# Kernel tuning notes

Hardware: AMD Instinct MI355X
Metric: run time of the kernel (lower is better)

The kernel has to match this reference:

```python
import jax, jax.numpy as jnp
import numpy as np

SAMPLES = 16        # samples per spatial dim -> M = SAMPLES**2 sample points
SAMPLE_PAD = 0
K = 9               # nearest neighbors == conv kernel size == stride


def setup_inputs() -> dict:
    key = jax.random.key(0)
    k1, k2, k3 = jax.random.split(key, 3)
    B, C, H, W = 16, 128, 64, 64
    OUT = 128
    x = jax.random.normal(k1, (B, C, H, W), dtype=jnp.float32)
    w = jax.random.normal(k2, (OUT, C, K), dtype=jnp.float32) * 0.05
    b = jax.random.normal(k3, (OUT,), dtype=jnp.float32) * 0.05
    return {"x": x, "w": w, "b": b}


def reference(x, w, b):
    B, C, H, W = x.shape
    N = H * W
    # --- spatial sample grid (static, shape-derived) ---
    xi = jnp.round(jnp.linspace(SAMPLE_PAD, H - SAMPLE_PAD - 1, SAMPLES)).astype(jnp.int32)
    yi = jnp.round(jnp.linspace(SAMPLE_PAD, W - SAMPLE_PAD - 1, SAMPLES)).astype(jnp.int32)
    xg, yg = jnp.meshgrid(xi, yi, indexing='ij')
    x_sample = x[:, :, xg, yg].reshape(B, C, -1)          # (B, C, M)
    x1 = x.reshape(B, C, N)                                # (B, C, N)
    # --- squared Euclidean distance between tokens and samples ---
    dots = jnp.einsum('bcn,bcm->bnm', x1, x_sample)        # (B, N, M)
    n2 = jnp.sum(x1 * x1, axis=1)                          # (B, N)
    m2 = jnp.sum(x_sample * x_sample, axis=1)              # (B, M)
    dist2 = n2[:, :, None] + m2[:, None, :] - 2.0 * dots   # (B, N, M)
    # K nearest samples per token (smallest distance)
    _, idx = jax.lax.top_k(-dist2, K)                      # (B, N, K) int32
    # gather neighbor features from the sample set: (B, C, N, K)
    nbrs = jnp.take_along_axis(x_sample[:, :, None, :],
                               idx[:, None, :, :], axis=3)
    # Conv1d(kernel=K, stride=K) over the (B, C, N*K) prime tensor
    out = jnp.einsum('bcnk,ock->bon', nbrs, w) + b[None, :, None]
    return out.reshape(B, w.shape[0], H, W)
```

## Files before the change

kernel.cpp:

```cpp
#include <hip/hip_runtime.h>

#define NB   16
#define NC   128
#define NN   4096
#define NM   256
#define NK   9
#define NO   128

typedef __attribute__((ext_vector_type(8))) short bf16x8;
typedef __attribute__((ext_vector_type(4))) float f32x4;

__device__ __constant__ int d_grid16[16] = {0,4,8,13,17,21,25,29,34,38,42,46,50,55,59,63};

__device__ inline unsigned short bf16_rne(float v) {
    unsigned u = __float_as_uint(v);
    return (unsigned short)((u + 0x7FFFu + ((u >> 16) & 1u)) >> 16);
}

__device__ __forceinline__ void merge16(unsigned* s, const unsigned* q) {
    unsigned r[16];
    #pragma unroll
    for (int i = 0; i < 16; ++i) r[i] = min(s[i], q[15 - i]);
    #pragma unroll
    for (int d = 8; d >= 1; d >>= 1)
        #pragma unroll
        for (int i = 0; i < 16; ++i)
            if (!(i & d)) { unsigned a = r[i], b2 = r[i + d]; r[i] = min(a, b2); r[i + d] = max(a, b2); }
    #pragma unroll
    for (int i = 0; i < 16; ++i) s[i] = r[i];
}

__global__ __launch_bounds__(256) void k_prep(const float* __restrict__ x,
                                              const float* __restrict__ w,
                                              float* __restrict__ xsT,
                                              unsigned short* __restrict__ xsTh,
                                              unsigned short* __restrict__ xsTl,
                                              unsigned short* __restrict__ Wth,
                                              unsigned short* __restrict__ Wtl,
                                              float* __restrict__ n2g,
                                              float* __restrict__ m2) {
    __shared__ float tile[16 * 260];
    int bx = blockIdx.x, t = threadIdx.x;
    if (bx < 128) {
        int b = bx >> 3, c0 = (bx & 7) * 16;
        int m = t;
        int pix = d_grid16[m >> 4] * 64 + d_grid16[m & 15];
        #pragma unroll
        for (int cc = 0; cc < 16; ++cc)
            tile[cc * 260 + m] = x[((size_t)b * NC + c0 + cc) * NN + pix];
        __syncthreads();
        #pragma unroll
        for (int e = 0; e < 4; ++e) {
            float fv[4];
            fv[0] = tile[(4 * e + 0) * 260 + m];
            fv[1] = tile[(4 * e + 1) * 260 + m];
            fv[2] = tile[(4 * e + 2) * 260 + m];
            fv[3] = tile[(4 * e + 3) * 260 + m];
            size_t base = ((size_t)b * NM + m) * NC + c0 + 4 * e;
            *(float4*)&xsT[base] = make_float4(fv[0], fv[1], fv[2], fv[3]);
            unsigned short h4[4], l4[4];
            #pragma unroll
            for (int e2 = 0; e2 < 4; ++e2) {
                unsigned short h = bf16_rne(fv[e2]);
                h4[e2] = h;
                l4[e2] = bf16_rne(fv[e2] - __uint_as_float(((unsigned)h) << 16));
            }
            *(ushort4*)&xsTh[base] = make_ushort4(h4[0], h4[1], h4[2], h4[3]);
            *(ushort4*)&xsTl[base] = make_ushort4(l4[0], l4[1], l4[2], l4[3]);
        }
    } else if (bx < 704) {
        int f = (bx - 128) * 256 + t;
        int ko = f >> 7, c = f & 127;
        int o = ko & 127, k = ko >> 7;
        float v = w[(size_t)o * 1152 + c * 9 + k];
        unsigned short h = bf16_rne(v);
        Wth[f] = h;
        Wtl[f] = bf16_rne(v - __uint_as_float(((unsigned)h) << 16));
    } else if (bx < 960) {
        #pragma clang fp contract(off)
        int i = bx - 704;
        int b = i >> 4, n = (i & 15) * 256 + t;
        const float* p = x + (size_t)b * NC * NN + n;
        float a = 0.f;
        #pragma unroll 16
        for (int c = 0; c < NC; ++c) { float v = p[(size_t)c * NN]; a = __fadd_rn(a, __fmul_rn(v, v)); }
        n2g[(size_t)b * NN + n] = a;
    } else {
        #pragma clang fp contract(off)
        int b = bx - 960;
        int pix = d_grid16[t >> 4] * 64 + d_grid16[t & 15];
        const float* p = x + (size_t)b * NC * NN + pix;
        float a = 0.f;
        #pragma unroll 16
        for (int c = 0; c < NC; ++c) { float v = p[(size_t)c * NN]; a = __fadd_rn(a, __fmul_rn(v, v)); }
        m2[b * NM + t] = a;
    }
}

__global__ __launch_bounds__(256) void k_g(const unsigned short* __restrict__ xsTh,
                                           const unsigned short* __restrict__ xsTl,
                                           const unsigned short* __restrict__ Wth,
                                           const unsigned short* __restrict__ Wtl,
                                           float* __restrict__ G) {
    int id = blockIdx.x;
    int b = id & 15, r = id >> 4;
    int kk = r % 9, q = r / 9;
    int mt = q >> 1, jh = q & 1;
    int t = threadIdx.x;
    int w = t >> 6, lane = t & 63;
    int lr = lane & 15, quad = lane >> 4;
    int m = b * NM + mt * 64 + w * 16 + lr;
    const unsigned short* aph = xsTh + (size_t)m * NC;
    const unsigned short* apl = xsTl + (size_t)m * NC;
    f32x4 acc[4];
    #pragma unroll
    for (int j = 0; j < 4; ++j) acc[j] = (f32x4){0.f, 0.f, 0.f, 0.f};
    #pragma unroll
    for (int kb = 0; kb < 4; ++kb) {
        int co = kb * 32 + quad * 8;
        bf16x8 Ah = *(const bf16x8*)&aph[co];
        bf16x8 Al = *(const bf16x8*)&apl[co];
        #pragma unroll
        for (int j = 0; j < 4; ++j) {
            size_t wrow = ((size_t)kk * 128 + jh * 64 + 16 * j + lr) * NC + co;
            bf16x8 Bh = *(const bf16x8*)&Wth[wrow];
            bf16x8 Bl = *(const bf16x8*)&Wtl[wrow];
            acc[j] = __builtin_amdgcn_mfma_f32_16x16x32_bf16(Ah, Bh, acc[j], 0, 0, 0);
            acc[j] = __builtin_amdgcn_mfma_f32_16x16x32_bf16(Al, Bh, acc[j], 0, 0, 0);
            acc[j] = __builtin_amdgcn_mfma_f32_16x16x32_bf16(Ah, Bl, acc[j], 0, 0, 0);
        }
    }
    int mrow = b * NM + mt * 64 + w * 16 + quad * 4;
    #pragma unroll
    for (int j = 0; j < 4; ++j)
        #pragma unroll
        for (int r2 = 0; r2 < 4; ++r2)
            G[((size_t)(mrow + r2)) * 1152 + kk * 128 + jh * 64 + 16 * j + lr] = acc[j][r2];
}

__global__ __launch_bounds__(256, 2) void k_sel(const float* __restrict__ x,
                                                const unsigned short* __restrict__ xsTh,
                                                const unsigned short* __restrict__ xsTl,
                                                const float* __restrict__ m2,
                                                int* __restrict__ idx) {
    __shared__ __align__(16) unsigned short xhp[32 * 136];
    __shared__ __align__(16) unsigned short xlp[32 * 136];
    __shared__ __align__(16) unsigned wl[2 * 4 * 16 * 16];
    __shared__ float m2l[256];

    int b = blockIdx.x & 15, n0 = (blockIdx.x >> 4) * 32;
    int t = threadIdx.x;
    int w = t >> 6, lane = t & 63;
    int lr = lane & 15, quad = lane >> 4;

    m2l[t] = m2[b * NM + t];

    #pragma unroll
    for (int it = 0; it < 4; ++it) {
        int f4 = it * 256 + t;
        int c = f4 >> 3, nn4 = (f4 & 7) * 4;
        float4 v = *(const float4*)&x[((size_t)b * NC + c) * NN + n0 + nn4];
        float vf[4] = {v.x, v.y, v.z, v.w};
        #pragma unroll
        for (int e = 0; e < 4; ++e) {
            unsigned short h = bf16_rne(vf[e]);
            unsigned short l = bf16_rne(vf[e] - __uint_as_float(((unsigned)h) << 16));
            xhp[(nn4 + e) * 136 + c] = h;
            xlp[(nn4 + e) * 136 + c] = l;
        }
    }
    __syncthreads();

    f32x4 acc[2][4];
    #pragma unroll
    for (int i = 0; i < 2; ++i)
        #pragma unroll
        for (int j = 0; j < 4; ++j) acc[i][j] = (f32x4){0.f, 0.f, 0.f, 0.f};
    int mbase = w * 64;
    #pragma unroll
    for (int kb = 0; kb < 4; ++kb) {
        int co = kb * 32 + quad * 8;
        bf16x8 Bh0 = *(const bf16x8*)&xhp[lr * 136 + co];
        bf16x8 Bl0 = *(const bf16x8*)&xlp[lr * 136 + co];
        bf16x8 Bh1 = *(const bf16x8*)&xhp[(16 + lr) * 136 + co];
        bf16x8 Bl1 = *(const bf16x8*)&xlp[(16 + lr) * 136 + co];
        bf16x8 Ah[4], Al[4];
        #pragma unroll
        for (int j = 0; j < 4; ++j) {
            size_t arow = ((size_t)(b * NM + mbase + 16 * j + lr)) * NC + co;
            Ah[j] = *(const bf16x8*)&xsTh[arow];
            Al[j] = *(const bf16x8*)&xsTl[arow];
        }
        #pragma unroll
        for (int j = 0; j < 4; ++j) {
            acc[0][j] = __builtin_amdgcn_mfma_f32_16x16x32_bf16(Ah[j], Bh0, acc[0][j], 0, 0, 0);
            acc[0][j] = __builtin_amdgcn_mfma_f32_16x16x32_bf16(Ah[j], Bl0, acc[0][j], 0, 0, 0);
            acc[0][j] = __builtin_amdgcn_mfma_f32_16x16x32_bf16(Al[j], Bh0, acc[0][j], 0, 0, 0);
            acc[1][j] = __builtin_amdgcn_mfma_f32_16x16x32_bf16(Ah[j], Bh1, acc[1][j], 0, 0, 0);
            acc[1][j] = __builtin_amdgcn_mfma_f32_16x16x32_bf16(Ah[j], Bl1, acc[1][j], 0, 0, 0);
            acc[1][j] = __builtin_amdgcn_mfma_f32_16x16x32_bf16(Al[j], Bh1, acc[1][j], 0, 0, 0);
        }
    }

    unsigned s16v[16];
    int hfirst = 1 - (w & 1);
    #pragma unroll
    for (int hh = 0; hh < 2; ++hh) {
        int h = (hh == 0) ? hfirst : 1 - hfirst;
        #pragma unroll
        for (int j = 0; j < 4; ++j)
            #pragma unroll
            for (int r = 0; r < 4; ++r) {
                int m = mbase + 16 * j + quad * 4 + r;
                float key = fmaf(-2.f, acc[h][j][r], m2l[m]);
                unsigned u = __float_as_uint(key);
                u = (u & 0x80000000u) ? ~u : (u | 0x80000000u);
                s16v[4 * j + r] = (u & 0xFFFFFF00u) | (unsigned)m;
            }
        #define CE(i,jx) { unsigned a_ = s16v[i], b_ = s16v[jx]; s16v[i] = min(a_, b_); s16v[jx] = max(a_, b_); }
        CE(0,1) CE(2,3) CE(0,2) CE(1,3) CE(1,2)
        CE(4,5) CE(6,7) CE(4,6) CE(5,7) CE(5,6)
        CE(0,4) CE(2,6) CE(2,4) CE(1,5) CE(3,7) CE(3,5) CE(1,2) CE(3,4) CE(5,6)
        CE(8,9) CE(10,11) CE(8,10) CE(9,11) CE(9,10)
        CE(12,13) CE(14,15) CE(12,14) CE(13,15) CE(13,14)
        CE(8,12) CE(10,14) CE(10,12) CE(9,13) CE(11,15) CE(11,13) CE(9,10) CE(11,12) CE(13,14)
        CE(0,8) CE(4,12) CE(4,8) CE(2,10) CE(6,14) CE(6,10) CE(2,4) CE(6,8) CE(10,12)
        CE(1,9) CE(5,13) CE(5,9) CE(3,11) CE(7,15) CE(7,11) CE(3,5) CE(7,9) CE(11,13)
        CE(1,2) CE(3,4) CE(5,6) CE(7,8) CE(9,10) CE(11,12) CE(13,14)
        #undef CE

        #pragma unroll
        for (int d = 16; d <= 32; d <<= 1) {
            unsigned q[16];
            #pragma unroll
            for (int i = 0; i < 16; ++i) q[i] = (unsigned)__shfl_xor((int)s16v[i], d, 64);
            merge16(s16v, q);
        }
        if (quad == 0) {
            #pragma unroll
            for (int ii = 0; ii < 4; ++ii)
                *(uint4*)&wl[(((h * 4 + w) * 16 + lr) * 16) + 4 * ii] =
                    make_uint4(s16v[4*ii], s16v[4*ii+1], s16v[4*ii+2], s16v[4*ii+3]);
        }
    }
    __syncthreads();

    if (w < 2) {
        int h = w;
        #pragma unroll
        for (int p = 1; p < 4; ++p) {
            int pw = (w + p) & 3;
            unsigned q[16];
            #pragma unroll
            for (int i = 0; i < 16; ++i) q[i] = wl[(((h * 4 + pw) * 16 + lr) * 16) + i];
            merge16(s16v, q);
        }
        if (quad == 0) {
            int tok = 16 * h + lr;
            size_t obase = (size_t)(b * NN + n0 + tok) * NK;
            #pragma unroll
            for (int i = 0; i < 4; ++i)
                idx[obase + i] = (int)((s16v[4*i] & 255u) | ((s16v[4*i+1] & 255u) << 8) |
                                       ((s16v[4*i+2] & 255u) << 16) | ((s16v[4*i+3] & 255u) << 24));
        }
    }
}

__global__ __launch_bounds__(256) void k_out(const float* __restrict__ x,
                                             const float* __restrict__ xsT,
                                             const float* __restrict__ m2,
                                             const float* __restrict__ n2g,
                                             const float* __restrict__ G,
                                             const int* __restrict__ idx,
                                             const float* __restrict__ bias,
                                             float* __restrict__ out) {
    #pragma clang fp contract(off)
    __shared__ __align__(16) unsigned char ubuf[33792];
    __shared__ unsigned long long pairs[64 * 17];
    __shared__ int   idxl[576];
    __shared__ float m2l[256];
    __shared__ float n2l[64];
    __shared__ float biasl[128];
    float* xr = (float*)ubuf;
    float* S  = (float*)ubuf;

    int b = blockIdx.x & 15, n0 = (blockIdx.x >> 4) * 64;
    int t = threadIdx.x;

    m2l[t] = m2[b * NM + t];
    if (t < 64)  n2l[t] = n2g[(size_t)b * NN + n0 + t];
    if (t < 128) biasl[t] = bias[t];

    int tok = t >> 2, grp = t & 3;
    unsigned candw = (unsigned)idx[(size_t)(b * NN + n0 + tok) * NK + grp];

    #pragma unroll
    for (int it = 0; it < 8; ++it) {
        int f4 = it * 256 + t;
        int c = f4 >> 4, nn4 = (f4 & 15) * 4;
        float4 v = *(const float4*)&x[((size_t)b * NC + c) * NN + n0 + nn4];
        xr[(nn4 + 0) * 132 + c] = v.x;
        xr[(nn4 + 1) * 132 + c] = v.y;
        xr[(nn4 + 2) * 132 + c] = v.z;
        xr[(nn4 + 3) * 132 + c] = v.w;
    }
    __syncthreads();

    {
        float n2 = n2l[tok];
        int mym[4];
        unsigned long long myp[4];
        #pragma unroll
        for (int s = 0; s < 4; ++s) {
            int m = (int)((candw >> (8 * s)) & 255u);
            mym[s] = m;
            const float* xt = xsT + ((size_t)(b * NM + m)) * NC;
            float dot = 0.f;
            for (int c4 = 0; c4 < 32; ++c4) {
                float4 xv = *(const float4*)&xr[tok * 132 + 4 * c4];
                float4 sv = *(const float4*)&xt[4 * c4];
                dot = __fadd_rn(dot, __fmul_rn(xv.x, sv.x));
                dot = __fadd_rn(dot, __fmul_rn(xv.y, sv.y));
                dot = __fadd_rn(dot, __fmul_rn(xv.z, sv.z));
                dot = __fadd_rn(dot, __fmul_rn(xv.w, sv.w));
            }
            float key = __fsub_rn(__fadd_rn(n2, m2l[m]), __fmul_rn(2.f, dot));
            unsigned u = __float_as_uint(key);
            u = (u & 0x80000000u) ? ~u : (u | 0x80000000u);
            myp[s] = ((unsigned long long)u << 32) | (unsigned)mym[s];
            pairs[tok * 17 + grp * 4 + s] = myp[s];
        }
        __syncthreads();
        unsigned long long pl[16];
        #pragma unroll
        for (int l2 = 0; l2 < 16; ++l2) pl[l2] = pairs[tok * 17 + l2];
        #pragma unroll
        for (int s = 0; s < 4; ++s) {
            int rank = 0;
            #pragma unroll
            for (int l2 = 0; l2 < 16; ++l2) rank += (pl[l2] < myp[s]);
            if (rank < 9) idxl[tok * 9 + rank] = mym[s];
        }
    }
    __syncthreads();

    {
        int o = t & 127, half = t >> 7;
        for (int p = 0; p < 32; ++p) {
            int n = p * 2 + half;
            float a = biasl[o];
            #pragma unroll
            for (int k = 0; k < 9; ++k) {
                int m = idxl[n * 9 + k];
                a += G[(((size_t)(b * NM + m)) * NK + k) * 128 + o];
            }
            S[n * 129 + o] = a;
        }
    }
    __syncthreads();

    {
        int nn = t & 63, ob = t >> 6;
        for (int p = 0; p < 32; ++p) {
            int o2 = p * 4 + ob;
            out[((size_t)(b * NO + o2)) * NN + n0 + nn] = S[nn * 129 + o2];
        }
    }
}

extern "C" void kernel_launch(void* const* d_in, const int* in_sizes, int n_in,
                              void* d_out, int out_size, void* d_ws, size_t ws_size,
                              hipStream_t stream) {
    const float* x    = (const float*)d_in[0];
    const float* w    = (const float*)d_in[1];
    const float* bias = (const float*)d_in[2];
    float* out = (float*)d_out;

    float* ws   = (float*)d_ws;
    float* m2   = ws;
    float* n2g  = ws + 4096;
    float* xsT  = ws + 69632;
    float* G    = ws + 593920;
    int*   idx  = (int*)(ws + 5312512);
    unsigned short* xsTh = (unsigned short*)(ws + 5902336);
    unsigned short* xsTl = (unsigned short*)(ws + 6164480);
    unsigned short* Wth  = (unsigned short*)(ws + 6426624);
    unsigned short* Wtl  = (unsigned short*)(ws + 6500352);

    k_prep<<<dim3(976),  dim3(256), 0, stream>>>(x, w, xsT, xsTh, xsTl, Wth, Wtl, n2g, m2);
    k_g   <<<dim3(1152), dim3(256), 0, stream>>>(xsTh, xsTl, Wth, Wtl, G);
    k_sel <<<dim3(2048), dim3(256), 0, stream>>>(x, xsTh, xsTl, m2, idx);
    k_out <<<dim3(1024), dim3(256), 0, stream>>>(x, xsT, m2, n2g, G, idx, bias, out);
}
```

Measured before the change: 266.3 us.

## Alias shared buffers, shuffle candidate exchange, unroll refine dot, raise k_out occupancy

In k_sel, the bf16 input planes and the warp merge buffer now share one LDS allocation, with a barrier added before the merge phase reuses it. This shrinks shared memory per block. In k_out, the 16 candidate pairs per token are exchanged with wave shuffles instead of an LDS array plus a barrier. The exact-precision dot loop is fully unrolled to batch its loads, and the launch bounds request 4 blocks per CU. The aim is more resident blocks and fewer syncs, at the risk of register pressure from the unrolling and the occupancy hint.

```diff
diff --git a/kernel.cpp b/kernel.cpp
--- a/kernel.cpp
+++ b/kernel.cpp
@@ -143,10 +143,11 @@
                                                 const unsigned short* __restrict__ xsTl,
                                                 const float* __restrict__ m2,
                                                 int* __restrict__ idx) {
-    __shared__ __align__(16) unsigned short xhp[32 * 136];
-    __shared__ __align__(16) unsigned short xlp[32 * 136];
-    __shared__ __align__(16) unsigned wl[2 * 4 * 16 * 16];
+    __shared__ __align__(16) unsigned short planes[2 * 32 * 136];
     __shared__ float m2l[256];
+    unsigned short* xhp = planes;
+    unsigned short* xlp = planes + 32 * 136;
+    unsigned* wl = (unsigned*)planes;
 
     int b = blockIdx.x & 15, n0 = (blockIdx.x >> 4) * 32;
     int t = threadIdx.x;
@@ -201,6 +202,7 @@
             acc[1][j] = __builtin_amdgcn_mfma_f32_16x16x32_bf16(Al[j], Bh1, acc[1][j], 0, 0, 0);
         }
     }
+    __syncthreads();
 
     unsigned s16v[16];
     int hfirst = 1 - (w & 1);
@@ -266,17 +268,16 @@
     }
 }
 
-__global__ __launch_bounds__(256) void k_out(const float* __restrict__ x,
-                                             const float* __restrict__ xsT,
-                                             const float* __restrict__ m2,
-                                             const float* __restrict__ n2g,
-                                             const float* __restrict__ G,
-                                             const int* __restrict__ idx,
-                                             const float* __restrict__ bias,
-                                             float* __restrict__ out) {
+__global__ __launch_bounds__(256, 4) void k_out(const float* __restrict__ x,
+                                                const float* __restrict__ xsT,
+                                                const float* __restrict__ m2,
+                                                const float* __restrict__ n2g,
+                                                const float* __restrict__ G,
+                                                const int* __restrict__ idx,
+                                                const float* __restrict__ bias,
+                                                float* __restrict__ out) {
     #pragma clang fp contract(off)
     __shared__ __align__(16) unsigned char ubuf[33792];
-    __shared__ unsigned long long pairs[64 * 17];
     __shared__ int   idxl[576];
     __shared__ float m2l[256];
     __shared__ float n2l[64];
@@ -310,30 +311,48 @@
         float n2 = n2l[tok];
         int mym[4];
         unsigned long long myp[4];
+        const float4* xr4 = (const float4*)&xr[tok * 132];
         #pragma unroll
         for (int s = 0; s < 4; ++s) {
             int m = (int)((candw >> (8 * s)) & 255u);
             mym[s] = m;
-            const float* xt = xsT + ((size_t)(b * NM + m)) * NC;
+            const float4* xt4 = (const float4*)(xsT + ((size_t)(b * NM + m)) * NC);
             float dot = 0.f;
-            for (int c4 = 0; c4 < 32; ++c4) {
-                float4 xv = *(const float4*)&xr[tok * 132 + 4 * c4];
-                float4 sv = *(const float4*)&xt[4 * c4];
-                dot = __fadd_rn(dot, __fmul_rn(xv.x, sv.x));
-                dot = __fadd_rn(dot, __fmul_rn(xv.y, sv.y));
-                dot = __fadd_rn(dot, __fmul_rn(xv.z, sv.z));
-                dot = __fadd_rn(dot, __fmul_rn(xv.w, sv.w));
+            #pragma unroll
+            for (int ep = 0; ep < 8; ++ep) {
+                float4 sv0 = xt4[ep * 4 + 0], sv1 = xt4[ep * 4 + 1];
+                float4 sv2 = xt4[ep * 4 + 2], sv3 = xt4[ep * 4 + 3];
+                float4 xv0 = xr4[ep * 4 + 0], xv1 = xr4[ep * 4 + 1];
+                float4 xv2 = xr4[ep * 4 + 2], xv3 = xr4[ep * 4 + 3];
+                dot = __fadd_rn(dot, __fmul_rn(xv0.x, sv0.x));
+                dot = __fadd_rn(dot, __fmul_rn(xv0.y, sv0.y));
+                dot = __fadd_rn(dot, __fmul_rn(xv0.z, sv0.z));
+                dot = __fadd_rn(dot, __fmul_rn(xv0.w, sv0.w));
+                dot = __fadd_rn(dot, __fmul_rn(xv1.x, sv1.x));
+                dot = __fadd_rn(dot, __fmul_rn(xv1.y, sv1.y));
+                dot = __fadd_rn(dot, __fmul_rn(xv1.z, sv1.z));
+                dot = __fadd_rn(dot, __fmul_rn(xv1.w, sv1.w));
+                dot = __fadd_rn(dot, __fmul_rn(xv2.x, sv2.x));
+                dot = __fadd_rn(dot, __fmul_rn(xv2.y, sv2.y));
+                dot = __fadd_rn(dot, __fmul_rn(xv2.z, sv2.z));
+                dot = __fadd_rn(dot, __fmul_rn(xv2.w, sv2.w));
+                dot = __fadd_rn(dot, __fmul_rn(xv3.x, sv3.x));
+                dot = __fadd_rn(dot, __fmul_rn(xv3.y, sv3.y));
+                dot = __fadd_rn(dot, __fmul_rn(xv3.z, sv3.z));
+                dot = __fadd_rn(dot, __fmul_rn(xv3.w, sv3.w));
             }
             float key = __fsub_rn(__fadd_rn(n2, m2l[m]), __fmul_rn(2.f, dot));
             unsigned u = __float_as_uint(key);
             u = (u & 0x80000000u) ? ~u : (u | 0x80000000u);
             myp[s] = ((unsigned long long)u << 32) | (unsigned)mym[s];
-            pairs[tok * 17 + grp * 4 + s] = myp[s];
-        }
-        __syncthreads();
+        }
         unsigned long long pl[16];
         #pragma unroll
-        for (int l2 = 0; l2 < 16; ++l2) pl[l2] = pairs[tok * 17 + l2];
+        for (int s = 0; s < 4; ++s) pl[s] = myp[s];
+        #pragma unroll
+        for (int s = 0; s < 4; ++s) pl[4 + s] = (unsigned long long)__shfl_xor((long long)pl[s], 1, 64);
+        #pragma unroll
+        for (int s = 0; s < 8; ++s) pl[8 + s] = (unsigned long long)__shfl_xor((long long)pl[s], 2, 64);
         #pragma unroll
         for (int s = 0; s < 4; ++s) {
             int rank = 0;
```

Measured after the change: 281.7 us. 5.8% more time.
